# Kernel tuning notes

Measured on AMD Instinct MI355X. Metric: run time of the kernel, lower is better.

The kernel has to match this reference:

```python
import jax, jax.numpy as jnp
import numpy as np

B, T, H, A, V, L = 4096, 16, 768, 128, 16, 2

def setup_inputs() -> dict:
    key = jax.random.key(0)
    ks = jax.random.split(key, 8)
    s = 0.02
    return {
        "last_hidden": jax.random.normal(ks[0], (B, T, H), jnp.float32),
        "attention_mask": jnp.ones((B, T), jnp.int64),
        "variety_ids": jax.random.randint(ks[1], (B,), 0, V),
        "Wd": jax.random.normal(ks[2], (V, H, A), jnp.float32) * s,  # per-variety down-proj
        "bd": jnp.zeros((V, A), jnp.float32),
        "Wu": jax.random.normal(ks[3], (V, A, H), jnp.float32) * s,  # per-variety up-proj
        "bu": jnp.zeros((V, H), jnp.float32),
        "Wc": jax.random.normal(ks[4], (L, H), jnp.float32) * s,     # classifier
        "bc": jnp.zeros((L,), jnp.float32),
    }

def reference(last_hidden, attention_mask, variety_ids, Wd, bd, Wu, bu, Wc, bc):
    x = last_hidden[:, 0, :]                                   # (B,H) CLS token
    # Dense grouped adapter: run all V bottleneck adapters, then select per example.
    h = jax.nn.gelu(jnp.einsum('bh,vha->bva', x, Wd) + bd[None])   # (B,V,A)
    u = jnp.einsum('bva,vah->bvh', h, Wu) + bu[None]               # (B,V,H)
    sel = u[jnp.arange(x.shape[0]), variety_ids]                   # (B,H) routed output
    adapted = x + sel                                              # residual bottleneck adapter
    # dropout is identity at p=0.0 / eval
    return adapted @ Wc.T + bc                                     # (B,L) logits
```

## Files before the change

### kernel.cpp

```cpp
#include <hip/hip_runtime.h>
#include <hip/hip_bf16.h>

#define BB 4096
#define TT 16
#define HH 768
#define AA 128
#define VV 16
#define LL 2

typedef __attribute__((ext_vector_type(8))) short short8v;
typedef __attribute__((ext_vector_type(4))) float float4v;

#define WS_OFFS 0
#define WS_ROWS 64
#define WS_WUC  4160
#define WS_BUC  8256
#define WS_ZBUF 8448

__device__ __forceinline__ unsigned short f2bf(float f) {
    __hip_bfloat16 h = __float2bfloat16(f);
    return *reinterpret_cast<unsigned short*>(&h);
}

__device__ __forceinline__ float gelu_tanh(float z) {
    float y = 0.7978845608028654f * (z + 0.044715f * z * z * z);
    y = fminf(fmaxf(y, -15.f), 15.f);
    float e = __expf(2.f * y);
    float th = (e - 1.f) / (e + 1.f);
    return 0.5f * z * (1.f + th);
}

__global__ __launch_bounds__(256) void k_prep(
    const int*   __restrict__ variety_ids,
    const float* __restrict__ Wu,
    const float* __restrict__ bu,
    const float* __restrict__ Wc,
    int* __restrict__ ws_i)
{
    const int t = threadIdx.x;
    if (blockIdx.x == 16) {
        __shared__ int hist[VV], hoff[VV + 1], hcur[VV];
        if (t < VV) hist[t] = 0;
        __syncthreads();
        for (int b = t; b < BB; b += 256) atomicAdd(&hist[variety_ids[b]], 1);
        __syncthreads();
        if (t == 0) {
            int s = 0;
            for (int i = 0; i < VV; ++i) { hoff[i] = s; s += hist[i]; }
            hoff[VV] = s;
            for (int i = 0; i <= VV; ++i) ws_i[WS_OFFS + i] = hoff[i];
        }
        __syncthreads();
        if (t < VV) hcur[t] = hoff[t];
        __syncthreads();
        for (int b = t; b < BB; b += 256) {
            int v = variety_ids[b];
            int p = atomicAdd(&hcur[v], 1);
            ws_i[WS_ROWS + p] = b;
        }
    } else {
        const int v = blockIdx.x;
        float* Wuc = (float*)(ws_i + WS_WUC);
        float* buc = (float*)(ws_i + WS_BUC);
        if (t < AA) {
            const float* wu = Wu + (size_t)v * AA * HH + (size_t)t * HH;
            float s0 = 0.f, s1 = 0.f;
            for (int h = 0; h < HH; h += 4) {
                float4 w  = *(const float4*)&wu[h];
                float4 c0 = *(const float4*)&Wc[h];
                float4 c1 = *(const float4*)&Wc[HH + h];
                s0 += w.x * c0.x + w.y * c0.y + w.z * c0.z + w.w * c0.w;
                s1 += w.x * c1.x + w.y * c1.y + w.z * c1.z + w.w * c1.w;
            }
            Wuc[(v * AA + t) * LL + 0] = s0;
            Wuc[(v * AA + t) * LL + 1] = s1;
        } else if (t < AA + LL) {
            const int l = t - AA;
            float s = 0.f;
            const float* bv = bu + (size_t)v * HH;
            for (int h = 0; h < HH; ++h) s += bv[h] * Wc[l * HH + h];
            buc[v * LL + l] = s;
        }
    }
}

__global__ __launch_bounds__(256) void k_down_mfma(
    const float* __restrict__ last_hidden,
    const float* __restrict__ Wd,
    const int*   __restrict__ ws_i,
    float* __restrict__ zbuf,
    int ks_count, int kslab)
{
    __shared__ __align__(16) unsigned short Xs[128 * 136];
    __shared__ __align__(16) unsigned short Wds[128 * 136];
    __shared__ int srows[128];

    const int* offs = ws_i + WS_OFFS;
    const int* rows = ws_i + WS_ROWS;
    const int t = threadIdx.x;

    const int bid = blockIdx.x;
    const int ks  = bid % ks_count;
    const int rt  = bid / ks_count;
    int v = -1, tloc = 0, cnt = 0, obase = 0, acc_t = 0;
    for (int vv = 0; vv < VV; ++vv) {
        int c  = offs[vv + 1] - offs[vv];
        int nt = (c + 127) >> 7;
        if (rt < acc_t + nt) {
            v = vv; tloc = rt - acc_t;
            cnt = c - tloc * 128; if (cnt > 128) cnt = 128;
            obase = offs[vv];
            break;
        }
        acc_t += nt;
    }
    if (v < 0) return;

    if (t < 128) {
        int rr = t < cnt ? t : cnt - 1;
        srows[t] = rows[obase + tloc * 128 + rr];
    }

    const int lane = t & 63;
    const int wv_  = t >> 6;
    const int wr = (wv_ >> 1) * 64, wc = (wv_ & 1) * 64;
    const int m = lane & 15, quad = lane >> 4;

    float4v acc[4][4];
    #pragma unroll
    for (int i = 0; i < 4; ++i)
        #pragma unroll
        for (int j = 0; j < 4; ++j)
            acc[i][j] = (float4v){0.f, 0.f, 0.f, 0.f};

    const float* wd = Wd + (size_t)v * HH * AA;
    const int nchunk = kslab >> 7;

    for (int kc = 0; kc < nchunk; ++kc) {
        const int ks0 = ks * kslab + kc * 128;
        __syncthreads();
        #pragma unroll
        for (int s = 0; s < 16; ++s) {
            int idx = t + s * 256;
            int r   = idx >> 5;
            int k4  = idx & 31;
            const float* xr = last_hidden + (size_t)srows[r] * TT * HH + ks0 + k4 * 4;
            float4 xv = *(const float4*)xr;
            unsigned int p0 = (unsigned)f2bf(xv.x) | ((unsigned)f2bf(xv.y) << 16);
            unsigned int p1 = (unsigned)f2bf(xv.z) | ((unsigned)f2bf(xv.w) << 16);
            *(uint2*)&Xs[r * 136 + k4 * 4] = make_uint2(p0, p1);
        }
        #pragma unroll
        for (int s = 0; s < 16; ++s) {
            int idx = t + s * 256;
            int hl  = idx >> 5;
            int a4  = idx & 31;
            float4 wv = *(const float4*)(wd + (size_t)(ks0 + hl) * AA + a4 * 4);
            Wds[(a4 * 4 + 0) * 136 + hl] = f2bf(wv.x);
            Wds[(a4 * 4 + 1) * 136 + hl] = f2bf(wv.y);
            Wds[(a4 * 4 + 2) * 136 + hl] = f2bf(wv.z);
            Wds[(a4 * 4 + 3) * 136 + hl] = f2bf(wv.w);
        }
        __syncthreads();

        #pragma unroll
        for (int k0 = 0; k0 < 128; k0 += 32) {
            short8v af[4], bf[4];
            #pragma unroll
            for (int i = 0; i < 4; ++i)
                af[i] = *(const short8v*)&Xs[(wr + i * 16 + m) * 136 + k0 + quad * 8];
            #pragma unroll
            for (int j = 0; j < 4; ++j)
                bf[j] = *(const short8v*)&Wds[(wc + j * 16 + m) * 136 + k0 + quad * 8];
            #pragma unroll
            for (int i = 0; i < 4; ++i)
                #pragma unroll
                for (int j = 0; j < 4; ++j)
                    acc[i][j] = __builtin_amdgcn_mfma_f32_16x16x32_bf16(af[i], bf[j], acc[i][j], 0, 0, 0);
        }
    }

    float* zs = zbuf + (size_t)ks * BB * AA;
    #pragma unroll
    for (int i = 0; i < 4; ++i) {
        #pragma unroll
        for (int reg = 0; reg < 4; ++reg) {
            int r = wr + i * 16 + quad * 4 + reg;
            if (r < cnt) {
                size_t base = (size_t)(obase + tloc * 128 + r) * AA;
                #pragma unroll
                for (int j = 0; j < 4; ++j)
                    zs[base + wc + j * 16 + m] = acc[i][j][reg];
            }
        }
    }
}

__global__ __launch_bounds__(256) void k_combine(
    const float* __restrict__ last_hidden,
    const int*   __restrict__ ws_i,
    const float* __restrict__ bd,
    const float* __restrict__ Wc,
    const float* __restrict__ bc,
    const float* __restrict__ zbuf,
    float* __restrict__ out,
    int ks_count)
{
    const int* offs = ws_i + WS_OFFS;
    const int* rows = ws_i + WS_ROWS;
    const float* Wuc = (const float*)(ws_i + WS_WUC);
    const float* buc = (const float*)(ws_i + WS_BUC);

    const int pos  = blockIdx.x * 4 + (threadIdx.x >> 6);
    const int lane = threadIdx.x & 63;
    const int gr = rows[pos];
    int v = 0;
    for (int vv = 0; vv < VV; ++vv)
        if (pos >= offs[vv] && pos < offs[vv + 1]) v = vv;

    const int a0 = lane * 2;
    float z0 = 0.f, z1 = 0.f;
    for (int ks = 0; ks < ks_count; ++ks) {
        float2 zz = *(const float2*)&zbuf[(size_t)ks * BB * AA + (size_t)pos * AA + a0];
        z0 += zz.x; z1 += zz.y;
    }
    z0 += bd[v * AA + a0];
    z1 += bd[v * AA + a0 + 1];
    float h0 = gelu_tanh(z0), h1 = gelu_tanh(z1);

    const float* wq = Wuc + (size_t)(v * AA + a0) * LL;
    float p0 = h0 * wq[0] + h1 * wq[2];
    float p1 = h0 * wq[1] + h1 * wq[3];

    const float* xr = last_hidden + (size_t)gr * TT * HH;
    #pragma unroll
    for (int s = 0; s < 12; ++s) {
        int h = lane + s * 64;
        float xv = xr[h];
        p0 += xv * Wc[h];
        p1 += xv * Wc[HH + h];
    }

    #pragma unroll
    for (int off = 32; off > 0; off >>= 1) {
        p0 += __shfl_down(p0, off);
        p1 += __shfl_down(p1, off);
    }
    if (lane == 0) {
        out[(size_t)gr * LL + 0] = p0 + bc[0] + buc[v * LL + 0];
        out[(size_t)gr * LL + 1] = p1 + bc[1] + buc[v * LL + 1];
    }
}

extern "C" void kernel_launch(void* const* d_in, const int* in_sizes, int n_in,
                              void* d_out, int out_size, void* d_ws, size_t ws_size,
                              hipStream_t stream) {
    const float* last_hidden = (const float*)d_in[0];
    const int*   variety_ids = (const int*)d_in[2];
    const float* Wd = (const float*)d_in[3];
    const float* bd = (const float*)d_in[4];
    const float* Wu = (const float*)d_in[5];
    const float* bu = (const float*)d_in[6];
    const float* Wc = (const float*)d_in[7];
    const float* bc = (const float*)d_in[8];
    float* out = (float*)d_out;

    int* ws_i = (int*)d_ws;
    float* zbuf = (float*)(ws_i + WS_ZBUF);

    size_t meta_bytes = (size_t)WS_ZBUF * 4;
    size_t slice = (size_t)BB * AA * 4;
    int KS = 6;
    if (ws_size < meta_bytes + 6 * slice) KS = 3;
    if (ws_size < meta_bytes + 3 * slice) KS = 2;
    if (ws_size < meta_bytes + 2 * slice) KS = 1;
    const int kslab = HH / KS;

    k_prep<<<17, 256, 0, stream>>>(variety_ids, Wu, bu, Wc, ws_i);
    k_down_mfma<<<48 * KS, 256, 0, stream>>>(last_hidden, Wd, ws_i, zbuf, KS, kslab);
    k_combine<<<BB / 4, 256, 0, stream>>>(last_hidden, ws_i, bd, Wc, bc, zbuf, out, KS);
}
```

Before: 299.4 us.

## Pre-convert Wd to transposed bf16 tiles in prep and parallelize prep reductions

The prep kernel now converts each variety's Wd slab to bf16 once, stores it in the workspace already transposed, and spreads the Wu·Wc and bu·Wc reductions across many more blocks with shared-memory partial sums. The down-projection kernel then loads pre-packed bf16 weight tiles with plain 16-byte copies instead of converting and transposing fp32 weights in every tile block, and the split count is fixed at 6 as a compile-time constant. This trades an extra workspace region and a heavier prep kernel for less redundant weight conversion and scattered LDS writes in the MFMA kernel. It assumes the workspace is large enough for six z slices plus the packed weights, because the fallback for smaller workspaces is gone.

```diff
diff --git a/kernel.cpp b/kernel.cpp
--- a/kernel.cpp
+++ b/kernel.cpp
@@ -7,6 +7,7 @@
 #define AA 128
 #define VV 16
 #define LL 2
+#define KS 6
 
 typedef __attribute__((ext_vector_type(8))) short short8v;
 typedef __attribute__((ext_vector_type(4))) float float4v;
@@ -15,7 +16,8 @@
 #define WS_ROWS 64
 #define WS_WUC  4160
 #define WS_BUC  8256
-#define WS_ZBUF 8448
+#define WS_WDP  8448
+#define WS_ZBUF (8448 + (VV * KS * AA * 128) / 2)
 
 __device__ __forceinline__ unsigned short f2bf(float f) {
     __hip_bfloat16 h = __float2bfloat16(f);
@@ -32,14 +34,85 @@
 
 __global__ __launch_bounds__(256) void k_prep(
     const int*   __restrict__ variety_ids,
+    const float* __restrict__ Wd,
     const float* __restrict__ Wu,
     const float* __restrict__ bu,
     const float* __restrict__ Wc,
     int* __restrict__ ws_i)
 {
+    __shared__ __align__(16) unsigned short Wds[128 * 136];
+    __shared__ float sp0[256], sp1[256];
+    __shared__ int hist[VV], hoff[VV + 1], hcur[VV];
+
     const int t = threadIdx.x;
-    if (blockIdx.x == 16) {
-        __shared__ int hist[VV], hoff[VV + 1], hcur[VV];
+    const int bid = blockIdx.x;
+    unsigned short* wdp = (unsigned short*)(ws_i + WS_WDP);
+    float* Wuc = (float*)(ws_i + WS_WUC);
+    float* buc = (float*)(ws_i + WS_BUC);
+
+    if (bid < 96) {
+        const int v = bid / KS, ks = bid % KS;
+        const float* wd = Wd + (size_t)v * HH * AA;
+        const int ks0 = ks * 128;
+        #pragma unroll
+        for (int s = 0; s < 16; ++s) {
+            int idx = t + s * 256;
+            int hl  = idx >> 5;
+            int a4  = idx & 31;
+            float4 wv = *(const float4*)(wd + (size_t)(ks0 + hl) * AA + a4 * 4);
+            Wds[(a4 * 4 + 0) * 136 + hl] = f2bf(wv.x);
+            Wds[(a4 * 4 + 1) * 136 + hl] = f2bf(wv.y);
+            Wds[(a4 * 4 + 2) * 136 + hl] = f2bf(wv.z);
+            Wds[(a4 * 4 + 3) * 136 + hl] = f2bf(wv.w);
+        }
+        __syncthreads();
+        unsigned short* dst = wdp + (size_t)(v * KS + ks) * AA * 128;
+        #pragma unroll
+        for (int s = 0; s < 8; ++s) {
+            int G = t + s * 256;
+            int a = G >> 4, g = G & 15;
+            uint4 w = *(const uint4*)&Wds[a * 136 + g * 8];
+            *(uint4*)&dst[a * 128 + g * 8] = w;
+        }
+    } else if (bid < 128) {
+        const int v  = (bid - 96) >> 1;
+        const int ah = (bid - 96) & 1;
+        const int a  = ah * 64 + (t >> 2);
+        const int q  = t & 3;
+        const float* wu = Wu + (size_t)v * AA * HH + (size_t)a * HH;
+        float s0 = 0.f, s1 = 0.f;
+        #pragma unroll 4
+        for (int h = q * 192; h < q * 192 + 192; h += 4) {
+            float4 w  = *(const float4*)&wu[h];
+            float4 c0 = *(const float4*)&Wc[h];
+            float4 c1 = *(const float4*)&Wc[HH + h];
+            s0 += w.x * c0.x + w.y * c0.y + w.z * c0.z + w.w * c0.w;
+            s1 += w.x * c1.x + w.y * c1.y + w.z * c1.z + w.w * c1.w;
+        }
+        sp0[t] = s0; sp1[t] = s1;
+        __syncthreads();
+        if (t < 64) {
+            float r0 = sp0[t * 4] + sp0[t * 4 + 1] + sp0[t * 4 + 2] + sp0[t * 4 + 3];
+            float r1 = sp1[t * 4] + sp1[t * 4 + 1] + sp1[t * 4 + 2] + sp1[t * 4 + 3];
+            int aa = ah * 64 + t;
+            Wuc[(v * AA + aa) * LL + 0] = r0;
+            Wuc[(v * AA + aa) * LL + 1] = r1;
+        }
+    } else if (bid == 128) {
+        const int pair = t >> 3, seg = t & 7;
+        const int v = pair >> 1, l = pair & 1;
+        float s = 0.f;
+        const float* bv = bu + (size_t)v * HH;
+        for (int h = seg * 96; h < seg * 96 + 96; ++h) s += bv[h] * Wc[l * HH + h];
+        sp0[t] = s;
+        __syncthreads();
+        if (t < 32) {
+            float r = 0.f;
+            #pragma unroll
+            for (int i = 0; i < 8; ++i) r += sp0[t * 8 + i];
+            buc[t] = r;
+        }
+    } else {
         if (t < VV) hist[t] = 0;
         __syncthreads();
         for (int b = t; b < BB; b += 256) atomicAdd(&hist[variety_ids[b]], 1);
@@ -58,38 +131,13 @@
             int p = atomicAdd(&hcur[v], 1);
             ws_i[WS_ROWS + p] = b;
         }
-    } else {
-        const int v = blockIdx.x;
-        float* Wuc = (float*)(ws_i + WS_WUC);
-        float* buc = (float*)(ws_i + WS_BUC);
-        if (t < AA) {
-            const float* wu = Wu + (size_t)v * AA * HH + (size_t)t * HH;
-            float s0 = 0.f, s1 = 0.f;
-            for (int h = 0; h < HH; h += 4) {
-                float4 w  = *(const float4*)&wu[h];
-                float4 c0 = *(const float4*)&Wc[h];
-                float4 c1 = *(const float4*)&Wc[HH + h];
-                s0 += w.x * c0.x + w.y * c0.y + w.z * c0.z + w.w * c0.w;
-                s1 += w.x * c1.x + w.y * c1.y + w.z * c1.z + w.w * c1.w;
-            }
-            Wuc[(v * AA + t) * LL + 0] = s0;
-            Wuc[(v * AA + t) * LL + 1] = s1;
-        } else if (t < AA + LL) {
-            const int l = t - AA;
-            float s = 0.f;
-            const float* bv = bu + (size_t)v * HH;
-            for (int h = 0; h < HH; ++h) s += bv[h] * Wc[l * HH + h];
-            buc[v * LL + l] = s;
-        }
     }
 }
 
 __global__ __launch_bounds__(256) void k_down_mfma(
     const float* __restrict__ last_hidden,
-    const float* __restrict__ Wd,
     const int*   __restrict__ ws_i,
-    float* __restrict__ zbuf,
-    int ks_count, int kslab)
+    float* __restrict__ zbuf)
 {
     __shared__ __align__(16) unsigned short Xs[128 * 136];
     __shared__ __align__(16) unsigned short Wds[128 * 136];
@@ -97,11 +145,11 @@
 
     const int* offs = ws_i + WS_OFFS;
     const int* rows = ws_i + WS_ROWS;
+    const unsigned short* wdp = (const unsigned short*)(ws_i + WS_WDP);
     const int t = threadIdx.x;
 
-    const int bid = blockIdx.x;
-    const int ks  = bid % ks_count;
-    const int rt  = bid / ks_count;
+    const int ks = blockIdx.x % KS;
+    const int rt = blockIdx.x / KS;
     int v = -1, tloc = 0, cnt = 0, obase = 0, acc_t = 0;
     for (int vv = 0; vv < VV; ++vv) {
         int c  = offs[vv + 1] - offs[vv];
@@ -120,6 +168,31 @@
         int rr = t < cnt ? t : cnt - 1;
         srows[t] = rows[obase + tloc * 128 + rr];
     }
+    __syncthreads();
+
+    const int ks0 = ks * 128;
+    #pragma unroll
+    for (int s = 0; s < 16; ++s) {
+        int idx = t + s * 256;
+        int r   = idx >> 5;
+        int k4  = idx & 31;
+        const float* xr = last_hidden + (size_t)srows[r] * TT * HH + ks0 + k4 * 4;
+        float4 xv = *(const float4*)xr;
+        unsigned int p0 = (unsigned)f2bf(xv.x) | ((unsigned)f2bf(xv.y) << 16);
+        unsigned int p1 = (unsigned)f2bf(xv.z) | ((unsigned)f2bf(xv.w) << 16);
+        *(uint2*)&Xs[r * 136 + k4 * 4] = make_uint2(p0, p1);
+    }
+    {
+        const unsigned short* wb = wdp + (size_t)(v * KS + ks) * AA * 128;
+        #pragma unroll
+        for (int s = 0; s < 8; ++s) {
+            int G = t + s * 256;
+            int a = G >> 4, g = G & 15;
+            uint4 w = *(const uint4*)&wb[a * 128 + g * 8];
+            *(uint4*)&Wds[a * 136 + g * 8] = w;
+        }
+    }
+    __syncthreads();
 
     const int lane = t & 63;
     const int wv_  = t >> 6;
@@ -133,51 +206,20 @@
         for (int j = 0; j < 4; ++j)
             acc[i][j] = (float4v){0.f, 0.f, 0.f, 0.f};
 
-    const float* wd = Wd + (size_t)v * HH * AA;
-    const int nchunk = kslab >> 7;
-
-    for (int kc = 0; kc < nchunk; ++kc) {
-        const int ks0 = ks * kslab + kc * 128;
-        __syncthreads();
-        #pragma unroll
-        for (int s = 0; s < 16; ++s) {
-            int idx = t + s * 256;
-            int r   = idx >> 5;
-            int k4  = idx & 31;
-            const float* xr = last_hidden + (size_t)srows[r] * TT * HH + ks0 + k4 * 4;
-            float4 xv = *(const float4*)xr;
-            unsigned int p0 = (unsigned)f2bf(xv.x) | ((unsigned)f2bf(xv.y) << 16);
-            unsigned int p1 = (unsigned)f2bf(xv.z) | ((unsigned)f2bf(xv.w) << 16);
-            *(uint2*)&Xs[r * 136 + k4 * 4] = make_uint2(p0, p1);
-        }
-        #pragma unroll
-        for (int s = 0; s < 16; ++s) {
-            int idx = t + s * 256;
-            int hl  = idx >> 5;
-            int a4  = idx & 31;
-            float4 wv = *(const float4*)(wd + (size_t)(ks0 + hl) * AA + a4 * 4);
-            Wds[(a4 * 4 + 0) * 136 + hl] = f2bf(wv.x);
-            Wds[(a4 * 4 + 1) * 136 + hl] = f2bf(wv.y);
-            Wds[(a4 * 4 + 2) * 136 + hl] = f2bf(wv.z);
-            Wds[(a4 * 4 + 3) * 136 + hl] = f2bf(wv.w);
-        }
-        __syncthreads();
-
-        #pragma unroll
-        for (int k0 = 0; k0 < 128; k0 += 32) {
-            short8v af[4], bf[4];
-            #pragma unroll
-            for (int i = 0; i < 4; ++i)
-                af[i] = *(const short8v*)&Xs[(wr + i * 16 + m) * 136 + k0 + quad * 8];
+    #pragma unroll
+    for (int k0 = 0; k0 < 128; k0 += 32) {
+        short8v af[4], bf[4];
+        #pragma unroll
+        for (int i = 0; i < 4; ++i)
+            af[i] = *(const short8v*)&Xs[(wr + i * 16 + m) * 136 + k0 + quad * 8];
+        #pragma unroll
+        for (int j = 0; j < 4; ++j)
+            bf[j] = *(const short8v*)&Wds[(wc + j * 16 + m) * 136 + k0 + quad * 8];
+        #pragma unroll
+        for (int i = 0; i < 4; ++i)
             #pragma unroll
             for (int j = 0; j < 4; ++j)
-                bf[j] = *(const short8v*)&Wds[(wc + j * 16 + m) * 136 + k0 + quad * 8];
-            #pragma unroll
-            for (int i = 0; i < 4; ++i)
-                #pragma unroll
-                for (int j = 0; j < 4; ++j)
-                    acc[i][j] = __builtin_amdgcn_mfma_f32_16x16x32_bf16(af[i], bf[j], acc[i][j], 0, 0, 0);
-        }
+                acc[i][j] = __builtin_amdgcn_mfma_f32_16x16x32_bf16(af[i], bf[j], acc[i][j], 0, 0, 0);
     }
 
     float* zs = zbuf + (size_t)ks * BB * AA;
@@ -203,8 +245,7 @@
     const float* __restrict__ Wc,
     const float* __restrict__ bc,
     const float* __restrict__ zbuf,
-    float* __restrict__ out,
-    int ks_count)
+    float* __restrict__ out)
 {
     const int* offs = ws_i + WS_OFFS;
     const int* rows = ws_i + WS_ROWS;
@@ -220,7 +261,8 @@
 
     const int a0 = lane * 2;
     float z0 = 0.f, z1 = 0.f;
-    for (int ks = 0; ks < ks_count; ++ks) {
+    #pragma unroll
+    for (int ks = 0; ks < KS; ++ks) {
         float2 zz = *(const float2*)&zbuf[(size_t)ks * BB * AA + (size_t)pos * AA + a0];
         z0 += zz.x; z1 += zz.y;
     }
@@ -268,15 +310,7 @@
     int* ws_i = (int*)d_ws;
     float* zbuf = (float*)(ws_i + WS_ZBUF);
 
-    size_t meta_bytes = (size_t)WS_ZBUF * 4;
-    size_t slice = (size_t)BB * AA * 4;
-    int KS = 6;
-    if (ws_size < meta_bytes + 6 * slice) KS = 3;
-    if (ws_size < meta_bytes + 3 * slice) KS = 2;
-    if (ws_size < meta_bytes + 2 * slice) KS = 1;
-    const int kslab = HH / KS;
-
-    k_prep<<<17, 256, 0, stream>>>(variety_ids, Wu, bu, Wc, ws_i);
-    k_down_mfma<<<48 * KS, 256, 0, stream>>>(last_hidden, Wd, ws_i, zbuf, KS, kslab);
-    k_combine<<<BB / 4, 256, 0, stream>>>(last_hidden, ws_i, bd, Wc, bc, zbuf, out, KS);
-}
+    k_prep<<<130, 256, 0, stream>>>(variety_ids, Wd, Wu, bu, Wc, ws_i);
+    k_down_mfma<<<48 * KS, 256, 0, stream>>>(last_hidden, ws_i, zbuf);
+    k_combine<<<BB / 4, 256, 0, stream>>>(last_hidden, ws_i, bd, Wc, bc, zbuf, out);
+}
```

Result: faster. 274.8 us (-8.2%).
